# Optimization experiments

Measured on AMD Instinct MI355X. Metric: run time of the kernel, lower is better.

## Reference

```python
import jax, jax.numpy as jnp
import numpy as np

D_OUT = 10          # number of classes (d_out)
TEMP = 1.0          # temperature T
EPS = 1e-07         # log eps from original code


def setup_inputs() -> dict:
    key = jax.random.key(0)
    k1, k2, k3, k4, k5 = jax.random.split(key, 5)
    N, M, d_in, dim = 2048, 131072, 128, 128
    x = jax.random.normal(k1, (N, d_in), dtype=jnp.float32)
    candidate_x = jax.random.normal(k2, (M, d_in), dtype=jnp.float32)
    candidate_y = jax.random.randint(k3, (M,), 0, D_OUT)
    # encoder = nn.Linear(d_in, dim): weight [dim, d_in], bias [dim]
    W = jax.random.normal(k4, (dim, d_in), dtype=jnp.float32) / np.float32(np.sqrt(d_in))
    b = jax.random.normal(k5, (dim,), dtype=jnp.float32) * 0.01
    return {"x": x, "candidate_x": candidate_x, "candidate_y": candidate_y, "W": W, "b": b}


def reference(x, candidate_x, candidate_y, W, b):
    # encoder (mode=0, n_blocks=0): single linear layer
    z = x @ W.T + b                 # [N, dim]
    zc = candidate_x @ W.T + b      # [M, dim]
    # torch.cdist(z, zc, p=2): pairwise euclidean distances [N, M]
    sq = (jnp.sum(z * z, axis=-1, keepdims=True)
          + jnp.sum(zc * zc, axis=-1)[None, :]
          - 2.0 * (z @ zc.T))
    dist = jnp.sqrt(jnp.maximum(sq, 1e-12)) / TEMP
    # is_train=False: no diagonal masking, no candidate subsampling
    probs = jax.nn.softmax(-dist, axis=-1)            # [N, M]
    onehot = jax.nn.one_hot(candidate_y, D_OUT, dtype=z.dtype)  # [M, D_OUT]
    logits = probs @ onehot                           # [N, D_OUT]
    return jnp.log(logits + EPS)
```

## Files before the change

### kernel.cpp

```cpp
#include <hip/hip_runtime.h>
#include <stdint.h>
#include <math.h>

#define N_ROWS 2048
#define M_CAND 131072
#define DIMK 128
#define DOUT 10
#define COLS_PER_BLOCK 1024
#define SUB_ITERS 16
#define CHUNKS_MAX 138
#define M_PAD_MAX (CHUNKS_MAX * COLS_PER_BLOCK)
#define LOG2E 1.4426950408889634f
#define L2E2 (LOG2E * LOG2E)

typedef __attribute__((ext_vector_type(8))) __bf16 bf16x8;
typedef __attribute__((ext_vector_type(8))) short s16x8;
typedef __attribute__((ext_vector_type(4))) float f32x4;
typedef __attribute__((ext_vector_type(2))) float f32x2;
typedef __attribute__((address_space(3))) void lds_void;
typedef const __attribute__((address_space(1))) void gbl_void;

__device__ __forceinline__ short f2bf(float f) {
  union { float f; unsigned u; } v; v.f = f;
  return (short)((v.u + 0x7fffu + ((v.u >> 16) & 1u)) >> 16);
}
__device__ __forceinline__ float bf2f(short h) {
  union { unsigned u; float f; } v;
  v.u = ((unsigned)(unsigned short)h) << 16; return v.f;
}
__device__ __forceinline__ float fast_sqrtf(float x) {
#if __has_builtin(__builtin_amdgcn_sqrtf)
  return __builtin_amdgcn_sqrtf(x);
#else
  return sqrtf(x);
#endif
}
__device__ __forceinline__ float fast_exp2f(float x) {
#if __has_builtin(__builtin_amdgcn_exp2f)
  return __builtin_amdgcn_exp2f(x);
#else
  return exp2f(x);
#endif
}

__device__ __forceinline__ void stage64(const short* gbase, short* lds, int t) {
  int w = t >> 6;
#pragma unroll
  for (int i = 0; i < 4; ++i) {
    int flat = i * 256 + t;
    int r = flat >> 4, s = flat & 15;
    int g = s ^ (r & 15);
    const short* src = gbase + r * DIMK + g * 8;
    short* dst = lds + (i * 256 + w * 64) * 8;
    __builtin_amdgcn_global_load_lds((gbl_void*)src, (lds_void*)dst, 16, 0, 0);
  }
}

__device__ __forceinline__ void mfma_tile(const short* As, const short* Bs,
                                          f32x4 acc[4][4], int wrow, int wcol,
                                          int quad, int l15) {
#pragma unroll
  for (int ks = 0; ks < 4; ++ks) {
    int slot = (ks * 4 + quad) ^ l15;
    bf16x8 a[4], b[4];
#pragma unroll
    for (int i = 0; i < 4; ++i) {
      a[i] = *(const bf16x8*)(As + (wrow + i * 16 + l15) * DIMK + slot * 8);
      b[i] = *(const bf16x8*)(Bs + (wcol + i * 16 + l15) * DIMK + slot * 8);
    }
#pragma unroll
    for (int i = 0; i < 4; ++i)
#pragma unroll
      for (int j = 0; j < 4; ++j)
        acc[i][j] = __builtin_amdgcn_mfma_f32_16x16x32_bf16(a[i], b[j], acc[i][j], 0, 0, 0);
  }
}

__global__ __launch_bounds__(256) void hist_kernel(const int* __restrict__ y,
                                                   int* __restrict__ cnt) {
  __shared__ int h[DOUT];
  int t = threadIdx.x;
  if (t < DOUT) h[t] = 0;
  __syncthreads();
  atomicAdd(&h[y[blockIdx.x * 256 + t]], 1);
  __syncthreads();
  if (t < DOUT) cnt[blockIdx.x * DOUT + t] = h[t];
}

__global__ __launch_bounds__(512) void scan_kernel(const int* __restrict__ cnt,
                                                   int* __restrict__ blockoff,
                                                   int* __restrict__ chunk_class,
                                                   int* __restrict__ invperm) {
  __shared__ int buf[2][512 * DOUT];
  __shared__ int pbnd[DOUT + 1];
  __shared__ int ccnt[DOUT];
  int t = threadIdx.x;
  int v[DOUT];
#pragma unroll
  for (int c = 0; c < DOUT; ++c) { v[c] = cnt[t * DOUT + c]; buf[0][t * DOUT + c] = v[c]; }
  __syncthreads();
  int src = 0;
  for (int off = 1; off < 512; off <<= 1) {
    int x[DOUT];
#pragma unroll
    for (int c = 0; c < DOUT; ++c) {
      x[c] = buf[src][t * DOUT + c];
      if (t >= off) x[c] += buf[src][(t - off) * DOUT + c];
    }
#pragma unroll
    for (int c = 0; c < DOUT; ++c) buf[1 - src][t * DOUT + c] = x[c];
    src ^= 1;
    __syncthreads();
  }
  if (t == 0) {
    int pb = 0;
    pbnd[0] = 0;
    for (int c = 0; c < DOUT; ++c) {
      int tot = buf[src][511 * DOUT + c];
      ccnt[c] = tot;
      pb += (tot + COLS_PER_BLOCK - 1) & ~(COLS_PER_BLOCK - 1);
      pbnd[c + 1] = pb;
    }
  }
  __syncthreads();
  if (t < CHUNKS_MAX) {
    int col = t * COLS_PER_BLOCK, c = 0;
#pragma unroll
    for (int k = 1; k < DOUT; ++k) c += (col >= pbnd[k]) ? 1 : 0;
    chunk_class[t] = c;
  }
  for (int c = 0; c < DOUT; ++c)
    for (int i = pbnd[c] + ccnt[c] + t; i < pbnd[c + 1]; i += 512) invperm[i] = -1;
  for (int i = pbnd[DOUT] + t; i < M_PAD_MAX; i += 512) invperm[i] = -1;
#pragma unroll
  for (int c = 0; c < DOUT; ++c)
    blockoff[t * DOUT + c] = pbnd[c] + buf[src][t * DOUT + c] - v[c];
}

__global__ __launch_bounds__(256) void scatter_kernel(const int* __restrict__ y,
                                                      const int* __restrict__ blockoff,
                                                      int* __restrict__ invperm) {
  __shared__ int cur[DOUT];
  int t = threadIdx.x;
  if (t < DOUT) cur[t] = blockoff[blockIdx.x * DOUT + t];
  __syncthreads();
  int e = blockIdx.x * 256 + t;
  int p = atomicAdd(&cur[y[e]], 1);
  invperm[p] = e;
}

__global__ __launch_bounds__(256, 2) void encoder_kernel(
    const float* __restrict__ X, const float* __restrict__ W,
    const float* __restrict__ bias, const int* __restrict__ invperm,
    short* __restrict__ Zb, float* __restrict__ Sq) {
  __shared__ __align__(16) short As[DIMK * DIMK];
  __shared__ __align__(16) short Bs[DIMK * DIMK];
  __shared__ float bias_s[DIMK];
  __shared__ float sqacc[DIMK];
  int t = threadIdx.x;
  int rowbase = blockIdx.x * 128;
  if (t < DIMK) { bias_s[t] = bias[t]; sqacc[t] = 0.f; }
#pragma unroll
  for (int i = 0; i < 8; ++i) {
    int flat = i * 256 + t;
    int r = flat >> 4, sl = flat & 15;
    int g = sl ^ (r & 15);
    const float* srcW = W + r * DIMK + g * 8;
    float4 a0 = *(const float4*)srcW;
    float4 a1 = *(const float4*)(srcW + 4);
    s16x8 wv;
    wv[0] = f2bf(a0.x); wv[1] = f2bf(a0.y); wv[2] = f2bf(a0.z); wv[3] = f2bf(a0.w);
    wv[4] = f2bf(a1.x); wv[5] = f2bf(a1.y); wv[6] = f2bf(a1.z); wv[7] = f2bf(a1.w);
    *(s16x8*)(Bs + r * DIMK + sl * 8) = wv;
    int xr = rowbase + r;
    int gxr = invperm ? invperm[xr] : xr;
    const float* srcX = X + (size_t)(gxr < 0 ? 0 : gxr) * DIMK + g * 8;
    float4 b0 = *(const float4*)srcX;
    float4 b1 = *(const float4*)(srcX + 4);
    if (gxr < 0) { b0 = make_float4(0.f, 0.f, 0.f, 0.f); b1 = b0; }
    s16x8 xv;
    xv[0] = f2bf(b0.x); xv[1] = f2bf(b0.y); xv[2] = f2bf(b0.z); xv[3] = f2bf(b0.w);
    xv[4] = f2bf(b1.x); xv[5] = f2bf(b1.y); xv[6] = f2bf(b1.z); xv[7] = f2bf(b1.w);
    *(s16x8*)(As + r * DIMK + sl * 8) = xv;
  }
  __syncthreads();
  int lane = t & 63, wid = t >> 6;
  int quad = lane >> 4, l15 = lane & 15;
  int wrow = (wid >> 1) * 64, wcol = (wid & 1) * 64;
  f32x4 acc[4][4];
  f32x4 z4 = {0.f, 0.f, 0.f, 0.f};
#pragma unroll
  for (int i = 0; i < 4; ++i)
#pragma unroll
    for (int j = 0; j < 4; ++j) acc[i][j] = z4;
  mfma_tile(As, Bs, acc, wrow, wcol, quad, l15);
#pragma unroll
  for (int ti = 0; ti < 4; ++ti) {
#pragma unroll
    for (int r = 0; r < 4; ++r) {
      int row_l = wrow + ti * 16 + quad * 4 + r;
      size_t grow = (size_t)(rowbase + row_l);
      float sqp = 0.f;
#pragma unroll
      for (int j = 0; j < 4; ++j) {
        int dcol = wcol + j * 16 + l15;
        float z = acc[ti][j][r] + bias_s[dcol];
        short hb = f2bf(z);
        float zr = bf2f(hb);
        sqp += zr * zr;
        Zb[grow * DIMK + dcol] = hb;
      }
      sqp += __shfl_xor(sqp, 1);
      sqp += __shfl_xor(sqp, 2);
      sqp += __shfl_xor(sqp, 4);
      sqp += __shfl_xor(sqp, 8);
      if (l15 == 0) atomicAdd(&sqacc[row_l], sqp);
    }
  }
  __syncthreads();
  if (t < DIMK) {
    bool dead = invperm && (invperm[rowbase + t] < 0);
    Sq[rowbase + t] = dead ? 1e30f : sqacc[t] * L2E2;
  }
}

__global__ __launch_bounds__(256, 4) void nca_main(
    const short* __restrict__ Zb, const short* __restrict__ Cb,
    const float* __restrict__ Sqz, const float* __restrict__ Sqc,
    float* __restrict__ partials) {
  __shared__ __align__(16) short Bs[2][64 * DIMK];
  __shared__ float sqc_s[COLS_PER_BLOCK];

  int t = threadIdx.x;
  int lane = t & 63, wid = t >> 6;
  int quad = lane >> 4, l15 = lane & 15;
  int wrow = wid * 32;
  int rowbase = blockIdx.x * 128;
  int colbase0 = blockIdx.y * COLS_PER_BLOCK;

  stage64(Cb + (size_t)colbase0 * DIMK, &Bs[0][0], t);

#pragma unroll
  for (int i = 0; i < 4; ++i)
    sqc_s[i * 256 + t] = Sqc[colbase0 + i * 256 + t];

  bf16x8 afrag[4][2];
#pragma unroll
  for (int ks = 0; ks < 4; ++ks)
#pragma unroll
    for (int ti = 0; ti < 2; ++ti)
      afrag[ks][ti] = *(const bf16x8*)(
          Zb + (size_t)(rowbase + wrow + ti * 16 + l15) * DIMK + ks * 32 + quad * 8);

  f32x2 szv2[2][2];
#pragma unroll
  for (int ti = 0; ti < 2; ++ti) {
    f32x4 s4 = *(const f32x4*)(Sqz + rowbase + wrow + ti * 16 + quad * 4);
    szv2[ti][0] = (f32x2){s4[0], s4[1]};
    szv2[ti][1] = (f32x2){s4[2], s4[3]};
  }

  float sum[8];
#pragma unroll
  for (int i = 0; i < 8; ++i) sum[i] = 0.f;

  const f32x2 m2 = {-2.0f * L2E2, -2.0f * L2E2};

  for (int it = 0; it < SUB_ITERS; ++it) {
    __syncthreads();
    if (it + 1 < SUB_ITERS)
      stage64(Cb + (size_t)(colbase0 + (it + 1) * 64) * DIMK, &Bs[(it + 1) & 1][0], t);
    const short* B = &Bs[it & 1][0];

    f32x4 acc[2][4];
    f32x4 z4 = {0.f, 0.f, 0.f, 0.f};
#pragma unroll
    for (int ti = 0; ti < 2; ++ti)
#pragma unroll
      for (int j = 0; j < 4; ++j) acc[ti][j] = z4;

#pragma unroll
    for (int ks = 0; ks < 4; ++ks) {
      int slot = (ks * 4 + quad) ^ l15;
      const short* p = B + l15 * DIMK + slot * 8;
      bf16x8 b0 = *(const bf16x8*)(p);
      bf16x8 b1 = *(const bf16x8*)(p + 16 * DIMK);
      bf16x8 b2 = *(const bf16x8*)(p + 32 * DIMK);
      bf16x8 b3 = *(const bf16x8*)(p + 48 * DIMK);
#pragma unroll
      for (int ti = 0; ti < 2; ++ti) {
        acc[ti][0] = __builtin_amdgcn_mfma_f32_16x16x32_bf16(afrag[ks][ti], b0, acc[ti][0], 0, 0, 0);
        acc[ti][1] = __builtin_amdgcn_mfma_f32_16x16x32_bf16(afrag[ks][ti], b1, acc[ti][1], 0, 0, 0);
        acc[ti][2] = __builtin_amdgcn_mfma_f32_16x16x32_bf16(afrag[ks][ti], b2, acc[ti][2], 0, 0, 0);
        acc[ti][3] = __builtin_amdgcn_mfma_f32_16x16x32_bf16(afrag[ks][ti], b3, acc[ti][3], 0, 0, 0);
      }
    }

    float sqcv[4];
#pragma unroll
    for (int j = 0; j < 4; ++j) sqcv[j] = sqc_s[it * 64 + j * 16 + l15];
#pragma unroll
    for (int ti = 0; ti < 2; ++ti)
#pragma unroll
      for (int j = 0; j < 4; ++j) {
        f32x2 q = {sqcv[j], sqcv[j]};
        f32x2 s01 = szv2[ti][0] + q;
        f32x2 s23 = szv2[ti][1] + q;
        f32x4 a = acc[ti][j];
        f32x2 a01 = {a[0], a[1]}, a23 = {a[2], a[3]};
        s01 = a01 * m2 + s01;
        s23 = a23 * m2 + s23;
        float e0 = fast_exp2f(-fast_sqrtf(__builtin_fabsf(s01[0])));
        float e1 = fast_exp2f(-fast_sqrtf(__builtin_fabsf(s01[1])));
        float e2 = fast_exp2f(-fast_sqrtf(__builtin_fabsf(s23[0])));
        float e3 = fast_exp2f(-fast_sqrtf(__builtin_fabsf(s23[1])));
        sum[ti * 4 + 0] += e0; sum[ti * 4 + 1] += e1;
        sum[ti * 4 + 2] += e2; sum[ti * 4 + 3] += e3;
      }
  }

#pragma unroll
  for (int si = 0; si < 8; ++si) {
    float s = sum[si];
    s += __shfl_xor(s, 1);
    s += __shfl_xor(s, 2);
    s += __shfl_xor(s, 4);
    s += __shfl_xor(s, 8);
    if (l15 == 0) {
      int row_l = wrow + (si >> 2) * 16 + quad * 4 + (si & 3);
      partials[(size_t)blockIdx.y * N_ROWS + rowbase + row_l] = s;
    }
  }
}

__global__ __launch_bounds__(64) void reduce_kernel(const float* __restrict__ partials,
                                                    const int* __restrict__ chunk_class,
                                                    float* __restrict__ out) {
  int row = blockIdx.x, lane = threadIdx.x;
  float s = 0.f;
  for (int ch = 0; ch < CHUNKS_MAX; ++ch) {
    float p = partials[(size_t)ch * N_ROWS + row];
    int c = chunk_class[ch];
    s += (lane == c) ? p : 0.f;
  }
  float tot = s;
  tot += __shfl_xor(tot, 1);
  tot += __shfl_xor(tot, 2);
  tot += __shfl_xor(tot, 4);
  tot += __shfl_xor(tot, 8);
  tot += __shfl_xor(tot, 16);
  tot += __shfl_xor(tot, 32);
  if (lane < DOUT)
    out[(size_t)row * DOUT + lane] = logf(s / tot + 1e-7f);
}

extern "C" void kernel_launch(void* const* d_in, const int* in_sizes, int n_in,
                              void* d_out, int out_size, void* d_ws, size_t ws_size,
                              hipStream_t stream) {
  const float* x = (const float*)d_in[0];
  const float* cx = (const float*)d_in[1];
  const int* cy = (const int*)d_in[2];
  const float* W = (const float*)d_in[3];
  const float* bias = (const float*)d_in[4];
  float* out = (float*)d_out;
  char* ws = (char*)d_ws;

  size_t off = 0;
  auto alloc = [&](size_t bytes) {
    void* p = ws + off;
    off = (off + bytes + 255) & ~(size_t)255;
    return p;
  };
  short* Zb = (short*)alloc((size_t)N_ROWS * DIMK * 2);
  short* Cb = (short*)alloc((size_t)M_PAD_MAX * DIMK * 2);
  float* Sqz = (float*)alloc((size_t)N_ROWS * 4);
  float* Sqc = (float*)alloc((size_t)M_PAD_MAX * 4);
  int* invperm = (int*)alloc((size_t)M_PAD_MAX * 4);
  int* cnt = (int*)alloc(512 * DOUT * 4);
  int* blockoff = (int*)alloc(512 * DOUT * 4);
  int* chunk_class = (int*)alloc(CHUNKS_MAX * 4);
  float* partials = (float*)alloc((size_t)CHUNKS_MAX * N_ROWS * 4);
  if (off > ws_size) return;

  hist_kernel<<<M_CAND / 256, 256, 0, stream>>>(cy, cnt);
  scan_kernel<<<1, 512, 0, stream>>>(cnt, blockoff, chunk_class, invperm);
  scatter_kernel<<<M_CAND / 256, 256, 0, stream>>>(cy, blockoff, invperm);
  encoder_kernel<<<N_ROWS / 128, 256, 0, stream>>>(x, W, bias, nullptr, Zb, Sqz);
  encoder_kernel<<<M_PAD_MAX / 128, 256, 0, stream>>>(cx, W, bias, invperm, Cb, Sqc);
  nca_main<<<dim3(N_ROWS / 128, CHUNKS_MAX), 256, 0, stream>>>(Zb, Cb, Sqz, Sqc, partials);
  reduce_kernel<<<N_ROWS, 64, 0, stream>>>(partials, chunk_class, out);
}
```

Measured before the change: 263.0 us.

## Restructure encoder with pre-converted bf16 W and register-resident X fragments

Adds a small kernel that converts W to bf16 once. A new encoder loads it into LDS with async global-to-LDS copies, and each wave loads its 16 X rows straight into MFMA A-fragments in registers, which removes the per-block fp32-to-bf16 conversion of W, the X staging through LDS and the shared-memory atomics for row norms. The main kernel now reads Sqc directly from global inside the loop instead of prefetching it into LDS, and accumulates its sums as packed float2. The cost is an extra kernel launch and uncoalesced per-lane X row reads.

```diff
diff --git a/kernel.cpp b/kernel.cpp
--- a/kernel.cpp
+++ b/kernel.cpp
@@ -20,6 +20,8 @@
 typedef __attribute__((address_space(3))) void lds_void;
 typedef const __attribute__((address_space(1))) void gbl_void;
 
+union frag_cast { s16x8 s; bf16x8 b; };
+
 __device__ __forceinline__ short f2bf(float f) {
   union { float f; unsigned u; } v; v.f = f;
   return (short)((v.u + 0x7fffu + ((v.u >> 16) & 1u)) >> 16);
@@ -56,23 +58,16 @@
   }
 }
 
-__device__ __forceinline__ void mfma_tile(const short* As, const short* Bs,
-                                          f32x4 acc[4][4], int wrow, int wcol,
-                                          int quad, int l15) {
-#pragma unroll
-  for (int ks = 0; ks < 4; ++ks) {
-    int slot = (ks * 4 + quad) ^ l15;
-    bf16x8 a[4], b[4];
-#pragma unroll
-    for (int i = 0; i < 4; ++i) {
-      a[i] = *(const bf16x8*)(As + (wrow + i * 16 + l15) * DIMK + slot * 8);
-      b[i] = *(const bf16x8*)(Bs + (wcol + i * 16 + l15) * DIMK + slot * 8);
-    }
-#pragma unroll
-    for (int i = 0; i < 4; ++i)
-#pragma unroll
-      for (int j = 0; j < 4; ++j)
-        acc[i][j] = __builtin_amdgcn_mfma_f32_16x16x32_bf16(a[i], b[j], acc[i][j], 0, 0, 0);
+__device__ __forceinline__ void stage128(const short* gbase, short* lds, int t) {
+  int w = t >> 6;
+#pragma unroll
+  for (int i = 0; i < 8; ++i) {
+    int flat = i * 256 + t;
+    int r = flat >> 4, s = flat & 15;
+    int g = s ^ (r & 15);
+    const short* src = gbase + r * DIMK + g * 8;
+    short* dst = lds + (i * 256 + w * 64) * 8;
+    __builtin_amdgcn_global_load_lds((gbl_void*)src, (lds_void*)dst, 16, 0, 0);
   }
 }
 
@@ -149,78 +144,89 @@
   invperm[p] = e;
 }
 
-__global__ __launch_bounds__(256, 2) void encoder_kernel(
-    const float* __restrict__ X, const float* __restrict__ W,
+__global__ __launch_bounds__(256) void convert_w_kernel(const float* __restrict__ W,
+                                                        short* __restrict__ Wb) {
+  int i = blockIdx.x * 256 + threadIdx.x;
+  Wb[i] = f2bf(W[i]);
+}
+
+__global__ __launch_bounds__(256, 4) void encoder2_kernel(
+    const float* __restrict__ X, const short* __restrict__ Wb,
     const float* __restrict__ bias, const int* __restrict__ invperm,
     short* __restrict__ Zb, float* __restrict__ Sq) {
-  __shared__ __align__(16) short As[DIMK * DIMK];
-  __shared__ __align__(16) short Bs[DIMK * DIMK];
-  __shared__ float bias_s[DIMK];
-  __shared__ float sqacc[DIMK];
-  int t = threadIdx.x;
-  int rowbase = blockIdx.x * 128;
-  if (t < DIMK) { bias_s[t] = bias[t]; sqacc[t] = 0.f; }
-#pragma unroll
-  for (int i = 0; i < 8; ++i) {
-    int flat = i * 256 + t;
-    int r = flat >> 4, sl = flat & 15;
-    int g = sl ^ (r & 15);
-    const float* srcW = W + r * DIMK + g * 8;
-    float4 a0 = *(const float4*)srcW;
-    float4 a1 = *(const float4*)(srcW + 4);
-    s16x8 wv;
-    wv[0] = f2bf(a0.x); wv[1] = f2bf(a0.y); wv[2] = f2bf(a0.z); wv[3] = f2bf(a0.w);
-    wv[4] = f2bf(a1.x); wv[5] = f2bf(a1.y); wv[6] = f2bf(a1.z); wv[7] = f2bf(a1.w);
-    *(s16x8*)(Bs + r * DIMK + sl * 8) = wv;
-    int xr = rowbase + r;
-    int gxr = invperm ? invperm[xr] : xr;
-    const float* srcX = X + (size_t)(gxr < 0 ? 0 : gxr) * DIMK + g * 8;
-    float4 b0 = *(const float4*)srcX;
-    float4 b1 = *(const float4*)(srcX + 4);
-    if (gxr < 0) { b0 = make_float4(0.f, 0.f, 0.f, 0.f); b1 = b0; }
-    s16x8 xv;
-    xv[0] = f2bf(b0.x); xv[1] = f2bf(b0.y); xv[2] = f2bf(b0.z); xv[3] = f2bf(b0.w);
-    xv[4] = f2bf(b1.x); xv[5] = f2bf(b1.y); xv[6] = f2bf(b1.z); xv[7] = f2bf(b1.w);
-    *(s16x8*)(As + r * DIMK + sl * 8) = xv;
-  }
-  __syncthreads();
+  __shared__ __align__(16) short Ws[DIMK * DIMK];
+  int t = threadIdx.x;
   int lane = t & 63, wid = t >> 6;
   int quad = lane >> 4, l15 = lane & 15;
-  int wrow = (wid >> 1) * 64, wcol = (wid & 1) * 64;
-  f32x4 acc[4][4];
-  f32x4 z4 = {0.f, 0.f, 0.f, 0.f};
-#pragma unroll
-  for (int i = 0; i < 4; ++i)
-#pragma unroll
-    for (int j = 0; j < 4; ++j) acc[i][j] = z4;
-  mfma_tile(As, Bs, acc, wrow, wcol, quad, l15);
-#pragma unroll
-  for (int ti = 0; ti < 4; ++ti) {
+  int rowbase = blockIdx.x * 64 + wid * 16;
+
+  stage128(Wb, Ws, t);
+
+  int grow = rowbase + l15;
+  int gxr = invperm ? invperm[grow] : grow;
+  bool dead = (gxr < 0);
+
+  bf16x8 afrag[4];
+#pragma unroll
+  for (int ks = 0; ks < 4; ++ks) {
+    frag_cast fc;
+    if (!dead) {
+      const float* p = X + (size_t)gxr * DIMK + ks * 32 + quad * 8;
+      float4 x0 = *(const float4*)p;
+      float4 x1 = *(const float4*)(p + 4);
+      fc.s[0] = f2bf(x0.x); fc.s[1] = f2bf(x0.y); fc.s[2] = f2bf(x0.z); fc.s[3] = f2bf(x0.w);
+      fc.s[4] = f2bf(x1.x); fc.s[5] = f2bf(x1.y); fc.s[6] = f2bf(x1.z); fc.s[7] = f2bf(x1.w);
+    } else {
+      fc.s = (s16x8){0, 0, 0, 0, 0, 0, 0, 0};
+    }
+    afrag[ks] = fc.b;
+  }
+
+  float bias_v[8];
+#pragma unroll
+  for (int j = 0; j < 8; ++j) bias_v[j] = bias[j * 16 + l15];
+
+  __syncthreads();
+
+  f32x4 acc[8];
+#pragma unroll
+  for (int j = 0; j < 8; ++j) acc[j] = (f32x4){0.f, 0.f, 0.f, 0.f};
+
+#pragma unroll
+  for (int ks = 0; ks < 4; ++ks) {
+    int slot = (ks * 4 + quad) ^ l15;
+    const short* p = Ws + l15 * DIMK + slot * 8;
+#pragma unroll
+    for (int j = 0; j < 8; ++j) {
+      bf16x8 b = *(const bf16x8*)(p + j * 16 * DIMK);
+      acc[j] = __builtin_amdgcn_mfma_f32_16x16x32_bf16(afrag[ks], b, acc[j], 0, 0, 0);
+    }
+  }
+
+  float sqp[4] = {0.f, 0.f, 0.f, 0.f};
+#pragma unroll
+  for (int j = 0; j < 8; ++j) {
 #pragma unroll
     for (int r = 0; r < 4; ++r) {
-      int row_l = wrow + ti * 16 + quad * 4 + r;
-      size_t grow = (size_t)(rowbase + row_l);
-      float sqp = 0.f;
-#pragma unroll
-      for (int j = 0; j < 4; ++j) {
-        int dcol = wcol + j * 16 + l15;
-        float z = acc[ti][j][r] + bias_s[dcol];
-        short hb = f2bf(z);
-        float zr = bf2f(hb);
-        sqp += zr * zr;
-        Zb[grow * DIMK + dcol] = hb;
-      }
-      sqp += __shfl_xor(sqp, 1);
-      sqp += __shfl_xor(sqp, 2);
-      sqp += __shfl_xor(sqp, 4);
-      sqp += __shfl_xor(sqp, 8);
-      if (l15 == 0) atomicAdd(&sqacc[row_l], sqp);
-    }
-  }
-  __syncthreads();
-  if (t < DIMK) {
-    bool dead = invperm && (invperm[rowbase + t] < 0);
-    Sq[rowbase + t] = dead ? 1e30f : sqacc[t] * L2E2;
+      float z = acc[j][r] + bias_v[j];
+      short hb = f2bf(z);
+      float zr = bf2f(hb);
+      sqp[r] = fmaf(zr, zr, sqp[r]);
+      Zb[(size_t)(rowbase + quad * 4 + r) * DIMK + j * 16 + l15] = hb;
+    }
+  }
+#pragma unroll
+  for (int r = 0; r < 4; ++r) {
+    float s = sqp[r];
+    s += __shfl_xor(s, 1);
+    s += __shfl_xor(s, 2);
+    s += __shfl_xor(s, 4);
+    s += __shfl_xor(s, 8);
+    if (l15 == 0) {
+      int row = rowbase + quad * 4 + r;
+      bool drow = invperm && (invperm[row] < 0);
+      Sq[row] = drow ? 1e30f : s * L2E2;
+    }
   }
 }
 
@@ -229,7 +235,6 @@
     const float* __restrict__ Sqz, const float* __restrict__ Sqc,
     float* __restrict__ partials) {
   __shared__ __align__(16) short Bs[2][64 * DIMK];
-  __shared__ float sqc_s[COLS_PER_BLOCK];
 
   int t = threadIdx.x;
   int lane = t & 63, wid = t >> 6;
@@ -240,10 +245,6 @@
 
   stage64(Cb + (size_t)colbase0 * DIMK, &Bs[0][0], t);
 
-#pragma unroll
-  for (int i = 0; i < 4; ++i)
-    sqc_s[i * 256 + t] = Sqc[colbase0 + i * 256 + t];
-
   bf16x8 afrag[4][2];
 #pragma unroll
   for (int ks = 0; ks < 4; ++ks)
@@ -260,16 +261,22 @@
     szv2[ti][1] = (f32x2){s4[2], s4[3]};
   }
 
-  float sum[8];
-#pragma unroll
-  for (int i = 0; i < 8; ++i) sum[i] = 0.f;
+  f32x2 sum2[4];
+#pragma unroll
+  for (int i = 0; i < 4; ++i) sum2[i] = (f32x2){0.f, 0.f};
 
   const f32x2 m2 = {-2.0f * L2E2, -2.0f * L2E2};
 
   for (int it = 0; it < SUB_ITERS; ++it) {
+    int colb = colbase0 + it * 64;
     __syncthreads();
+
+    float sqcv[4];
+#pragma unroll
+    for (int j = 0; j < 4; ++j) sqcv[j] = Sqc[colb + j * 16 + l15];
+
     if (it + 1 < SUB_ITERS)
-      stage64(Cb + (size_t)(colbase0 + (it + 1) * 64) * DIMK, &Bs[(it + 1) & 1][0], t);
+      stage64(Cb + (size_t)(colb + 64) * DIMK, &Bs[(it + 1) & 1][0], t);
     const short* B = &Bs[it & 1][0];
 
     f32x4 acc[2][4];
@@ -296,9 +303,6 @@
       }
     }
 
-    float sqcv[4];
-#pragma unroll
-    for (int j = 0; j < 4; ++j) sqcv[j] = sqc_s[it * 64 + j * 16 + l15];
 #pragma unroll
     for (int ti = 0; ti < 2; ++ti)
 #pragma unroll
@@ -314,14 +318,14 @@
         float e1 = fast_exp2f(-fast_sqrtf(__builtin_fabsf(s01[1])));
         float e2 = fast_exp2f(-fast_sqrtf(__builtin_fabsf(s23[0])));
         float e3 = fast_exp2f(-fast_sqrtf(__builtin_fabsf(s23[1])));
-        sum[ti * 4 + 0] += e0; sum[ti * 4 + 1] += e1;
-        sum[ti * 4 + 2] += e2; sum[ti * 4 + 3] += e3;
+        sum2[ti * 2 + 0] += (f32x2){e0, e1};
+        sum2[ti * 2 + 1] += (f32x2){e2, e3};
       }
   }
 
 #pragma unroll
   for (int si = 0; si < 8; ++si) {
-    float s = sum[si];
+    float s = sum2[si >> 1][si & 1];
     s += __shfl_xor(s, 1);
     s += __shfl_xor(s, 2);
     s += __shfl_xor(s, 4);
@@ -373,6 +377,7 @@
   };
   short* Zb = (short*)alloc((size_t)N_ROWS * DIMK * 2);
   short* Cb = (short*)alloc((size_t)M_PAD_MAX * DIMK * 2);
+  short* Wb = (short*)alloc((size_t)DIMK * DIMK * 2);
   float* Sqz = (float*)alloc((size_t)N_ROWS * 4);
   float* Sqc = (float*)alloc((size_t)M_PAD_MAX * 4);
   int* invperm = (int*)alloc((size_t)M_PAD_MAX * 4);
@@ -385,8 +390,9 @@
   hist_kernel<<<M_CAND / 256, 256, 0, stream>>>(cy, cnt);
   scan_kernel<<<1, 512, 0, stream>>>(cnt, blockoff, chunk_class, invperm);
   scatter_kernel<<<M_CAND / 256, 256, 0, stream>>>(cy, blockoff, invperm);
-  encoder_kernel<<<N_ROWS / 128, 256, 0, stream>>>(x, W, bias, nullptr, Zb, Sqz);
-  encoder_kernel<<<M_PAD_MAX / 128, 256, 0, stream>>>(cx, W, bias, invperm, Cb, Sqc);
+  convert_w_kernel<<<DIMK * DIMK / 256, 256, 0, stream>>>(W, Wb);
+  encoder2_kernel<<<N_ROWS / 64, 256, 0, stream>>>(x, Wb, bias, nullptr, Zb, Sqz);
+  encoder2_kernel<<<M_PAD_MAX / 64, 256, 0, stream>>>(cx, Wb, bias, invperm, Cb, Sqc);
   nca_main<<<dim3(N_ROWS / 128, CHUNKS_MAX), 256, 0, stream>>>(Zb, Cb, Sqz, Sqc, partials);
   reduce_kernel<<<N_ROWS, 64, 0, stream>>>(partials, chunk_class, out);
 }
```

After: 246.1 us. 6.4% less time.
